# Kernel optimization log

Hardware: AMD Instinct MI355X
Metric: run time of the kernel (lower is better)

## Reference

```python
import jax, jax.numpy as jnp
import numpy as np

D = 256          # out_feats
H = 4            # n_heads
DH = D // H      # per-head feats
S = 8192         # number of snapshots (segments)
PER = 32         # edges (selected papers) per snapshot
E = S * PER      # total edges
NP = 200000      # number of papers
ST = 10          # snapshot_types (embedding has ST+1 rows, padding_idx=-1)
SLOPE = 0.01     # LeakyReLU negative slope (torch default)


def setup_inputs() -> dict:
    key = jax.random.key(0)
    ks = jax.random.split(key, 20)
    sc = 1.0 / np.sqrt(D)
    papers = jax.random.normal(ks[0], (NP, D), dtype=jnp.float32)
    snapshots = jax.random.normal(ks[1], (S, D), dtype=jnp.float32)
    cur_snapshot_types = jax.random.randint(ks[2], (S,), 0, ST + 1, dtype=jnp.int32)
    is_cite = jax.random.randint(ks[3], (NP,), 0, 2, dtype=jnp.int32)
    selected_indicator = jax.random.randint(ks[4], (E,), 0, NP, dtype=jnp.int64)
    # contiguous sorted segment ids, PER edges per snapshot (matches valid_num_nodes)
    index = jnp.repeat(jnp.arange(S, dtype=jnp.int32), PER)
    # linear layers (torch Linear: y = x @ W.T + b)
    W_src = jax.random.normal(ks[5], (D, D), dtype=jnp.float32) * sc
    b_src = jnp.zeros((D,), dtype=jnp.float32)
    W_dst = jax.random.normal(ks[6], (D, D), dtype=jnp.float32) * sc
    b_dst = jnp.zeros((D,), dtype=jnp.float32)
    W_out = jax.random.normal(ks[7], (D, D), dtype=jnp.float32) * sc
    b_out = jnp.zeros((D,), dtype=jnp.float32)
    # node attr embeddings (2 rows, padding_idx=0 -> row 0 zero)
    emb_cite = jax.random.normal(ks[8], (2, D), dtype=jnp.float32).at[0].set(0.0)
    emb_ref = jax.random.normal(ks[9], (2, D), dtype=jnp.float32).at[0].set(0.0)
    emb_target = jax.random.normal(ks[10], (2, D), dtype=jnp.float32).at[0].set(0.0)
    # snapshot type embedding (ST+1 rows, padding_idx=-1 -> last row zero)
    snapshot_emb = jax.random.normal(ks[11], (ST + 1, D), dtype=jnp.float32).at[-1].set(0.0)
    # attention vectors, xavier_normal with relu gain
    gain = np.sqrt(2.0)
    std = gain * np.sqrt(2.0 / (H * DH + 1))
    attn = jax.random.normal(ks[12], (1, H, DH), dtype=jnp.float32) * std
    attn_t = jax.random.normal(ks[13], (1, H, DH), dtype=jnp.float32) * std
    return {
        "papers": papers, "snapshots": snapshots,
        "W_src": W_src, "b_src": b_src, "W_dst": W_dst, "b_dst": b_dst,
        "W_out": W_out, "b_out": b_out,
        "emb_cite": emb_cite, "emb_ref": emb_ref, "emb_target": emb_target,
        "snapshot_emb": snapshot_emb, "attn": attn, "attn_t": attn_t,
        "cur_snapshot_types": cur_snapshot_types, "is_cite": is_cite,
        "selected_indicator": selected_indicator, "index": index,
    }


def _leaky(x):
    return jnp.where(x >= 0, x, SLOPE * x)


def reference(papers, snapshots, W_src, b_src, W_dst, b_dst, W_out, b_out,
              emb_cite, emb_ref, emb_target, snapshot_emb, attn, attn_t,
              cur_snapshot_types, is_cite, selected_indicator, index):
    # gather src papers per edge: [E, D]
    h_src = papers[selected_indicator]
    feat_src = (h_src @ W_src.T + b_src).reshape(-1, H, DH)          # [E,H,DH]
    ic = is_cite[selected_indicator]
    # original uses 'is_cite' indices for all three attr embeddings (faithful)
    src_type_h = (emb_cite[ic] + emb_ref[ic] + emb_target[ic]).reshape(-1, H, DH)
    dst_type_h = snapshot_emb[cur_snapshot_types].reshape(-1, H, DH)  # [S,H,DH]
    feat_dst = (snapshots @ W_dst.T + b_dst).reshape(-1, H, DH)[index]  # [E,H,DH]
    # per-edge attention logits
    e = (_leaky(feat_src + feat_dst) * attn).sum(axis=-1)             # [E,H]
    et = (_leaky(src_type_h + dst_type_h[index]) * attn_t).sum(axis=-1)
    e = e + et
    # segment (edge) softmax over destination snapshots
    m = jax.lax.stop_gradient(jax.ops.segment_max(e, index, num_segments=S))
    ex = jnp.exp(e - m[index])
    den = jax.ops.segment_sum(ex, index, num_segments=S)
    a = (ex / den[index])[..., None]                                  # [E,H,1]
    # weighted segment-sum aggregation
    x = feat_src * a
    sum_out = jax.ops.segment_sum(x, index, num_segments=S).reshape(S, D)
    return sum_out @ W_out.T + b_out
```

## Files before the change

kernel.cpp:

```cpp
#include <hip/hip_runtime.h>
#include <hip/hip_fp16.h>
#include <type_traits>

#define NSNAP 8192
#define PER 32
#define SLOPE 0.01f

using half8   = __attribute__((ext_vector_type(8))) _Float16;
using floatx4 = __attribute__((ext_vector_type(4))) float;

__device__ __forceinline__ float leaky(float x) { return x >= 0.f ? x : SLOPE * x; }

__device__ __forceinline__ unsigned pack2(float a, float b) {
    __half2 h = __floats2half2_rn(a, b);
    return *reinterpret_cast<unsigned*>(&h);
}

__global__ __launch_bounds__(256) void pack_w_frag(const float* __restrict__ W,
                                                   _Float16* __restrict__ Wh) {
    const int t = blockIdx.x * 256 + threadIdx.x;
    const int lane = t & 63;
    const int wj = (t >> 6) & 15;
    const int k0 = t >> 10;
    const int n = (wj >> 2) * 64 + (wj & 3) * 16 + (lane & 15);
    const int k = k0 * 32 + (lane >> 4) * 8;
    const float4 v0 = *(const float4*)(W + (long)n * 256 + k);
    const float4 v1 = *(const float4*)(W + (long)n * 256 + k + 4);
    *(uint4*)(Wh + (long)t * 8) =
        make_uint4(pack2(v0.x, v0.y), pack2(v0.z, v0.w), pack2(v1.x, v1.y), pack2(v1.z, v1.w));
}

template <typename AT, typename OT>
__global__ __launch_bounds__(256) void gemm_nt(const AT* __restrict__ A,
                                               const float* __restrict__ W,
                                               const float* __restrict__ bias,
                                               OT* __restrict__ Cout, int M) {
    constexpr int LDA = 40;
    __shared__ _Float16 Asl[128 * LDA];
    __shared__ _Float16 Wsl[128 * LDA];

    const int m0 = blockIdx.x * 128;
    const int n0 = blockIdx.y * 128;
    const int tid = threadIdx.x;
    const int lane = tid & 63;
    const int wave = tid >> 6;
    const int wm = (wave & 1) * 64;
    const int wn = (wave >> 1) * 64;
    const int l15 = lane & 15;
    const int quad = lane >> 4;

    floatx4 acc[4][4];
#pragma unroll
    for (int i = 0; i < 4; i++)
#pragma unroll
        for (int j = 0; j < 4; j++) acc[i][j] = (floatx4)0.f;

    for (int k0 = 0; k0 < 256; k0 += 32) {
        __syncthreads();
#pragma unroll
        for (int it = 0; it < 4; ++it) {
            const int idx = tid + it * 256;
            const int row = idx >> 3;
            const int c4 = idx & 7;
            long gm = (long)m0 + row;
            if (gm >= M) gm = M - 1;
            if constexpr (std::is_same_v<AT, float>) {
                const float4 v = *(const float4*)(A + gm * 256 + k0 + c4 * 4);
                *(uint2*)(&Asl[row * LDA + c4 * 4]) = make_uint2(pack2(v.x, v.y), pack2(v.z, v.w));
            } else {
                const uint2 v = *(const uint2*)(A + gm * 256 + k0 + c4 * 4);
                *(uint2*)(&Asl[row * LDA + c4 * 4]) = v;
            }
            const float4 w = *(const float4*)(W + (long)(n0 + row) * 256 + k0 + c4 * 4);
            *(uint2*)(&Wsl[row * LDA + c4 * 4]) = make_uint2(pack2(w.x, w.y), pack2(w.z, w.w));
        }
        __syncthreads();

        half8 af[4], bf[4];
#pragma unroll
        for (int i = 0; i < 4; i++)
            af[i] = *reinterpret_cast<const half8*>(&Asl[(wm + i * 16 + l15) * LDA + quad * 8]);
#pragma unroll
        for (int j = 0; j < 4; j++)
            bf[j] = *reinterpret_cast<const half8*>(&Wsl[(wn + j * 16 + l15) * LDA + quad * 8]);
#pragma unroll
        for (int i = 0; i < 4; i++)
#pragma unroll
            for (int j = 0; j < 4; j++)
                acc[i][j] = __builtin_amdgcn_mfma_f32_16x16x32_f16(af[i], bf[j], acc[i][j], 0, 0, 0);
    }

#pragma unroll
    for (int j = 0; j < 4; j++) {
        const int gcol = n0 + wn + j * 16 + l15;
        const float bv = bias[gcol];
#pragma unroll
        for (int i = 0; i < 4; i++) {
            const int rbase = m0 + wm + i * 16 + quad * 4;
#pragma unroll
            for (int r = 0; r < 4; r++) {
                const int grow = rbase + r;
                if (grow < M) {
                    const float v = acc[i][j][r] + bv;
                    if constexpr (std::is_same_v<OT, __half>)
                        Cout[(long)grow * 256 + gcol] = __float2half(v);
                    else
                        Cout[(long)grow * 256 + gcol] = v;
                }
            }
        }
    }
}

__global__ __launch_bounds__(256, 2) void fused_attn(
    const float* __restrict__ papers, const _Float16* __restrict__ Wh,
    const float* __restrict__ b_src, const float* __restrict__ F,
    const float* __restrict__ emb_cite, const float* __restrict__ emb_ref,
    const float* __restrict__ emb_target, const float* __restrict__ snap_emb,
    const float* __restrict__ attn, const float* __restrict__ attn_t,
    const int* __restrict__ types, const int* __restrict__ is_cite,
    const int* __restrict__ sel, __half* __restrict__ SO) {
    __shared__ _Float16 Asl[64 * 256];
    __shared__ int ic_l[64];

    const int tid = threadIdx.x;
    const int lane = tid & 63;
    const int wave = tid >> 6;
    const int l15 = lane & 15;
    const int quad = lane >> 4;
    const int sbase = blockIdx.x * 2;
    const int ebase = blockIdx.x * 64;

    if (tid < 64) ic_l[tid] = is_cite[sel[ebase + tid]];

    {
        const int r = tid >> 2;
        const int q0 = tid & 3;
        const long arow = (long)sel[ebase + r];
        const float* src = papers + arow * 256 + q0 * 64;
        const int i = r >> 4;
        const int rl = r & 15;
#pragma unroll
        for (int m = 0; m < 8; m++) {
            const float4 a0 = *(const float4*)(src + m * 8);
            const float4 a1 = *(const float4*)(src + m * 8 + 4);
            const int c8 = q0 * 8 + m;
            const int addr8 = (c8 >> 2) * 256 + i * 64 + (c8 & 3) * 16 + rl;
            *(uint4*)(&Asl[addr8 * 8]) = make_uint4(pack2(a0.x, a0.y), pack2(a0.z, a0.w),
                                                    pack2(a1.x, a1.y), pack2(a1.z, a1.w));
        }
    }
    __syncthreads();

    floatx4 acc[4][4];
#pragma unroll
    for (int i = 0; i < 4; i++)
#pragma unroll
        for (int j = 0; j < 4; j++) acc[i][j] = (floatx4)0.f;

    for (int k0 = 0; k0 < 8; k0++) {
        half8 af[4], bf[4];
#pragma unroll
        for (int i = 0; i < 4; i++)
            af[i] = *reinterpret_cast<const half8*>(&Asl[(k0 * 256 + i * 64 + lane) * 8]);
#pragma unroll
        for (int j = 0; j < 4; j++)
            bf[j] = *reinterpret_cast<const half8*>(Wh + ((k0 * 16 + wave * 4 + j) * 64 + lane) * 8);
#pragma unroll
        for (int i = 0; i < 4; i++)
#pragma unroll
            for (int j = 0; j < 4; j++)
                acc[i][j] = __builtin_amdgcn_mfma_f32_16x16x32_f16(af[i], bf[j], acc[i][j], 0, 0, 0);
    }

    float bsrc_j[4], attn_j[4], F0_j[4], F1_j[4];
#pragma unroll
    for (int j = 0; j < 4; j++) {
        const int col = 64 * wave + j * 16 + l15;
        bsrc_j[j] = b_src[col];
        attn_j[j] = attn[col];
        F0_j[j] = F[(long)sbase * 256 + col];
        F1_j[j] = F[(long)(sbase + 1) * 256 + col];
    }
#pragma unroll
    for (int i = 0; i < 4; i++)
#pragma unroll
        for (int j = 0; j < 4; j++)
#pragma unroll
            for (int r = 0; r < 4; r++) acc[i][j][r] += bsrc_j[j];

    const int D = 64 * wave + lane;
    const float at_d = attn_t[D];
    const float src0 = emb_cite[D] + emb_ref[D] + emb_target[D];
    const float src1 = emb_cite[256 + D] + emb_ref[256 + D] + emb_target[256 + D];
    float et[2][2];
#pragma unroll
    for (int sn = 0; sn < 2; sn++) {
        const float dstt = snap_emb[types[sbase + sn] * 256 + D];
        float p0 = leaky(src0 + dstt) * at_d;
        float p1 = leaky(src1 + dstt) * at_d;
#pragma unroll
        for (int off = 32; off; off >>= 1) {
            p0 += __shfl_xor(p0, off);
            p1 += __shfl_xor(p1, off);
        }
        et[sn][0] = p0;
        et[sn][1] = p1;
    }

    float lg[4][4];
#pragma unroll
    for (int i = 0; i < 4; i++) {
        const int sn = i >> 1;
#pragma unroll
        for (int r = 0; r < 4; r++) {
            float p = 0.f;
#pragma unroll
            for (int j = 0; j < 4; j++)
                p += leaky(acc[i][j][r] + (sn == 0 ? F0_j[j] : F1_j[j])) * attn_j[j];
#pragma unroll
            for (int off = 1; off <= 8; off <<= 1) p += __shfl_xor(p, off);
            const int row = i * 16 + quad * 4 + r;
            lg[i][r] = p + et[sn][ic_l[row]];
        }
    }

    float aw[4][4];
#pragma unroll
    for (int sn = 0; sn < 2; sn++) {
        float m = -3.4e38f;
#pragma unroll
        for (int ii = 0; ii < 2; ii++)
#pragma unroll
            for (int r = 0; r < 4; r++) m = fmaxf(m, lg[sn * 2 + ii][r]);
        m = fmaxf(m, __shfl_xor(m, 16));
        m = fmaxf(m, __shfl_xor(m, 32));
        float den = 0.f;
#pragma unroll
        for (int ii = 0; ii < 2; ii++)
#pragma unroll
            for (int r = 0; r < 4; r++) {
                const float ex = __expf(lg[sn * 2 + ii][r] - m);
                aw[sn * 2 + ii][r] = ex;
                den += ex;
            }
        den += __shfl_xor(den, 16);
        den += __shfl_xor(den, 32);
        const float inv = 1.f / den;
#pragma unroll
        for (int ii = 0; ii < 2; ii++)
#pragma unroll
            for (int r = 0; r < 4; r++) aw[sn * 2 + ii][r] *= inv;
    }

#pragma unroll
    for (int sn = 0; sn < 2; sn++) {
#pragma unroll
        for (int j = 0; j < 4; j++) {
            float o = 0.f;
#pragma unroll
            for (int ii = 0; ii < 2; ii++)
#pragma unroll
                for (int r = 0; r < 4; r++) o += aw[sn * 2 + ii][r] * acc[sn * 2 + ii][j][r];
            o += __shfl_xor(o, 16);
            o += __shfl_xor(o, 32);
            if (quad == sn)
                SO[(long)(sbase + sn) * 256 + 64 * wave + j * 16 + l15] = __float2half(o);
        }
    }
}

extern "C" void kernel_launch(void* const* d_in, const int* in_sizes, int n_in,
                              void* d_out, int out_size, void* d_ws, size_t ws_size,
                              hipStream_t stream) {
    const float* papers     = (const float*)d_in[0];
    const float* snapshots  = (const float*)d_in[1];
    const float* W_src      = (const float*)d_in[2];
    const float* b_src      = (const float*)d_in[3];
    const float* W_dst      = (const float*)d_in[4];
    const float* b_dst      = (const float*)d_in[5];
    const float* W_out      = (const float*)d_in[6];
    const float* b_out      = (const float*)d_in[7];
    const float* emb_cite   = (const float*)d_in[8];
    const float* emb_ref    = (const float*)d_in[9];
    const float* emb_target = (const float*)d_in[10];
    const float* snap_emb   = (const float*)d_in[11];
    const float* attn       = (const float*)d_in[12];
    const float* attn_t     = (const float*)d_in[13];
    const int* types        = (const int*)d_in[14];
    const int* is_cite      = (const int*)d_in[15];
    const int* sel          = (const int*)d_in[16];

    char* ws = (char*)d_ws;
    float*     F    = (float*)ws;
    __half*    SO   = (__half*)(ws + 8388608);
    _Float16*  Wh   = (_Float16*)(ws + 12582912);

    pack_w_frag<<<128, 256, 0, stream>>>(W_src, Wh);
    gemm_nt<float, float><<<dim3(64, 2), 256, 0, stream>>>(snapshots, W_dst, b_dst, F, NSNAP);
    fused_attn<<<NSNAP / 2, 256, 0, stream>>>(papers, Wh, b_src, F, emb_cite, emb_ref,
                                              emb_target, snap_emb, attn, attn_t, types,
                                              is_cite, sel, SO);
    gemm_nt<__half, float><<<dim3(64, 2), 256, 0, stream>>>(SO, W_out, b_out, (float*)d_out, NSNAP);
}
```

Before: 404.9 us.

## Shrink GEMM tiles to 64x64, fold weight packing into GEMM launch, recoalesce gather

The dense GEMMs switch from 128x128 tiles on a 64x2 grid to 64x64 tiles on a 128x4 grid, quadrupling block count so more of the GPU's compute units are busy. The W_src fp16 fragment packing moves into an extra grid row of the first GEMM, removing one kernel launch. The paper-row gather in the fused attention kernel is remapped so each wave loads 16 rows with lanes reading consecutive float4s. Smaller tiles reuse less data per block, and the M-bound guards are removed, which assumes M is a multiple of 64.

After: 386.8 us. 4.5% less time.

```diff
diff --git a/kernel.cpp b/kernel.cpp
--- a/kernel.cpp
+++ b/kernel.cpp
@@ -16,59 +16,60 @@
     return *reinterpret_cast<unsigned*>(&h);
 }
 
-__global__ __launch_bounds__(256) void pack_w_frag(const float* __restrict__ W,
-                                                   _Float16* __restrict__ Wh) {
-    const int t = blockIdx.x * 256 + threadIdx.x;
-    const int lane = t & 63;
-    const int wj = (t >> 6) & 15;
-    const int k0 = t >> 10;
-    const int n = (wj >> 2) * 64 + (wj & 3) * 16 + (lane & 15);
-    const int k = k0 * 32 + (lane >> 4) * 8;
-    const float4 v0 = *(const float4*)(W + (long)n * 256 + k);
-    const float4 v1 = *(const float4*)(W + (long)n * 256 + k + 4);
-    *(uint4*)(Wh + (long)t * 8) =
-        make_uint4(pack2(v0.x, v0.y), pack2(v0.z, v0.w), pack2(v1.x, v1.y), pack2(v1.z, v1.w));
-}
-
-template <typename AT, typename OT>
-__global__ __launch_bounds__(256) void gemm_nt(const AT* __restrict__ A,
-                                               const float* __restrict__ W,
-                                               const float* __restrict__ bias,
-                                               OT* __restrict__ Cout, int M) {
+template <typename AT, typename OT, bool DO_PACK>
+__global__ __launch_bounds__(256) void gemm64(const AT* __restrict__ A,
+                                              const float* __restrict__ W,
+                                              const float* __restrict__ bias,
+                                              OT* __restrict__ Cout, int M,
+                                              const float* __restrict__ Wsrc,
+                                              _Float16* __restrict__ Wh) {
+    if constexpr (DO_PACK) {
+        if (blockIdx.y == 4) {
+            const int t = blockIdx.x * 256 + threadIdx.x;
+            const int lane = t & 63;
+            const int wj = (t >> 6) & 15;
+            const int k0 = t >> 10;
+            const int n = (wj >> 2) * 64 + (wj & 3) * 16 + (lane & 15);
+            const int k = k0 * 32 + (lane >> 4) * 8;
+            const float4 v0 = *(const float4*)(Wsrc + (long)n * 256 + k);
+            const float4 v1 = *(const float4*)(Wsrc + (long)n * 256 + k + 4);
+            *(uint4*)(Wh + (long)t * 8) = make_uint4(pack2(v0.x, v0.y), pack2(v0.z, v0.w),
+                                                     pack2(v1.x, v1.y), pack2(v1.z, v1.w));
+            return;
+        }
+    }
     constexpr int LDA = 40;
-    __shared__ _Float16 Asl[128 * LDA];
-    __shared__ _Float16 Wsl[128 * LDA];
-
-    const int m0 = blockIdx.x * 128;
-    const int n0 = blockIdx.y * 128;
+    __shared__ _Float16 Asl[64 * LDA];
+    __shared__ _Float16 Wsl[64 * LDA];
+
+    const int m0 = blockIdx.x * 64;
+    const int n0 = blockIdx.y * 64;
     const int tid = threadIdx.x;
     const int lane = tid & 63;
     const int wave = tid >> 6;
-    const int wm = (wave & 1) * 64;
-    const int wn = (wave >> 1) * 64;
+    const int wm = (wave & 1) * 32;
+    const int wn = (wave >> 1) * 32;
     const int l15 = lane & 15;
     const int quad = lane >> 4;
 
-    floatx4 acc[4][4];
-#pragma unroll
-    for (int i = 0; i < 4; i++)
-#pragma unroll
-        for (int j = 0; j < 4; j++) acc[i][j] = (floatx4)0.f;
+    floatx4 acc[2][2];
+#pragma unroll
+    for (int i = 0; i < 2; i++)
+#pragma unroll
+        for (int j = 0; j < 2; j++) acc[i][j] = (floatx4)0.f;
 
     for (int k0 = 0; k0 < 256; k0 += 32) {
         __syncthreads();
 #pragma unroll
-        for (int it = 0; it < 4; ++it) {
+        for (int it = 0; it < 2; ++it) {
             const int idx = tid + it * 256;
             const int row = idx >> 3;
             const int c4 = idx & 7;
-            long gm = (long)m0 + row;
-            if (gm >= M) gm = M - 1;
             if constexpr (std::is_same_v<AT, float>) {
-                const float4 v = *(const float4*)(A + gm * 256 + k0 + c4 * 4);
+                const float4 v = *(const float4*)(A + (long)(m0 + row) * 256 + k0 + c4 * 4);
                 *(uint2*)(&Asl[row * LDA + c4 * 4]) = make_uint2(pack2(v.x, v.y), pack2(v.z, v.w));
             } else {
-                const uint2 v = *(const uint2*)(A + gm * 256 + k0 + c4 * 4);
+                const uint2 v = *(const uint2*)(A + (long)(m0 + row) * 256 + k0 + c4 * 4);
                 *(uint2*)(&Asl[row * LDA + c4 * 4]) = v;
             }
             const float4 w = *(const float4*)(W + (long)(n0 + row) * 256 + k0 + c4 * 4);
@@ -76,37 +77,34 @@
         }
         __syncthreads();
 
-        half8 af[4], bf[4];
-#pragma unroll
-        for (int i = 0; i < 4; i++)
+        half8 af[2], bf[2];
+#pragma unroll
+        for (int i = 0; i < 2; i++)
             af[i] = *reinterpret_cast<const half8*>(&Asl[(wm + i * 16 + l15) * LDA + quad * 8]);
 #pragma unroll
-        for (int j = 0; j < 4; j++)
+        for (int j = 0; j < 2; j++)
             bf[j] = *reinterpret_cast<const half8*>(&Wsl[(wn + j * 16 + l15) * LDA + quad * 8]);
 #pragma unroll
-        for (int i = 0; i < 4; i++)
-#pragma unroll
-            for (int j = 0; j < 4; j++)
+        for (int i = 0; i < 2; i++)
+#pragma unroll
+            for (int j = 0; j < 2; j++)
                 acc[i][j] = __builtin_amdgcn_mfma_f32_16x16x32_f16(af[i], bf[j], acc[i][j], 0, 0, 0);
     }
 
 #pragma unroll
-    for (int j = 0; j < 4; j++) {
+    for (int j = 0; j < 2; j++) {
         const int gcol = n0 + wn + j * 16 + l15;
         const float bv = bias[gcol];
 #pragma unroll
-        for (int i = 0; i < 4; i++) {
+        for (int i = 0; i < 2; i++) {
             const int rbase = m0 + wm + i * 16 + quad * 4;
 #pragma unroll
             for (int r = 0; r < 4; r++) {
-                const int grow = rbase + r;
-                if (grow < M) {
-                    const float v = acc[i][j][r] + bv;
-                    if constexpr (std::is_same_v<OT, __half>)
-                        Cout[(long)grow * 256 + gcol] = __float2half(v);
-                    else
-                        Cout[(long)grow * 256 + gcol] = v;
-                }
+                const float v = acc[i][j][r] + bv;
+                if constexpr (std::is_same_v<OT, __half>)
+                    Cout[(long)(rbase + r) * 256 + gcol] = __float2half(v);
+                else
+                    Cout[(long)(rbase + r) * 256 + gcol] = v;
             }
         }
     }
@@ -134,20 +132,16 @@
     if (tid < 64) ic_l[tid] = is_cite[sel[ebase + tid]];
 
     {
-        const int r = tid >> 2;
-        const int q0 = tid & 3;
-        const long arow = (long)sel[ebase + r];
-        const float* src = papers + arow * 256 + q0 * 64;
-        const int i = r >> 4;
-        const int rl = r & 15;
-#pragma unroll
-        for (int m = 0; m < 8; m++) {
-            const float4 a0 = *(const float4*)(src + m * 8);
-            const float4 a1 = *(const float4*)(src + m * 8 + 4);
-            const int c8 = q0 * 8 + m;
-            const int addr8 = (c8 >> 2) * 256 + i * 64 + (c8 & 3) * 16 + rl;
-            *(uint4*)(&Asl[addr8 * 8]) = make_uint4(pack2(a0.x, a0.y), pack2(a0.z, a0.w),
-                                                    pack2(a1.x, a1.y), pack2(a1.z, a1.w));
+        const int row = wave * 16 + l15;
+        const long arow = (long)sel[ebase + row];
+        const float* src = papers + arow * 256;
+#pragma unroll
+        for (int m = 0; m < 16; m++) {
+            const float4 v = *(const float4*)(src + m * 16 + quad * 4);
+            const int c8 = m * 2 + (quad >> 1);
+            const int slot = (c8 >> 2) * 256 + wave * 64 + (c8 & 3) * 16 + l15;
+            *(uint2*)(&Asl[slot * 8 + (quad & 1) * 4]) =
+                make_uint2(pack2(v.x, v.y), pack2(v.z, v.w));
         }
     }
     __syncthreads();
@@ -296,10 +290,12 @@
     __half*    SO   = (__half*)(ws + 8388608);
     _Float16*  Wh   = (_Float16*)(ws + 12582912);
 
-    pack_w_frag<<<128, 256, 0, stream>>>(W_src, Wh);
-    gemm_nt<float, float><<<dim3(64, 2), 256, 0, stream>>>(snapshots, W_dst, b_dst, F, NSNAP);
+    gemm64<float, float, true><<<dim3(128, 5), 256, 0, stream>>>(snapshots, W_dst, b_dst, F,
+                                                                 NSNAP, W_src, Wh);
     fused_attn<<<NSNAP / 2, 256, 0, stream>>>(papers, Wh, b_src, F, emb_cite, emb_ref,
                                               emb_target, snap_emb, attn, attn_t, types,
                                               is_cite, sel, SO);
-    gemm_nt<__half, float><<<dim3(64, 2), 256, 0, stream>>>(SO, W_out, b_out, (float*)d_out, NSNAP);
+    gemm64<__half, float, false><<<dim3(128, 4), 256, 0, stream>>>(SO, W_out, b_out,
+                                                                   (float*)d_out, NSNAP,
+                                                                   nullptr, nullptr);
 }
```
